# Kernel tuning notes

Measured on AMD Instinct MI355X. Metric: run time of the kernel, lower is better.

The kernel has to match this reference:

```python
import jax, jax.numpy as jnp
import numpy as np

N_NODES = 20000
N_EDGES = 320000
N_ADJ = 4
D = 256
CSTR = [0, 1]          # constrained adjacency subset for the last step
RATIO = 1.0
LN_EPS = 1e-5


def setup_inputs() -> dict:
    key = jax.random.key(0)
    ks = jax.random.split(key, 10)
    x = jax.random.normal(ks[0], (N_NODES, D), dtype=jnp.float32)
    rows = jax.random.randint(ks[1], (N_ADJ, N_EDGES), 0, N_NODES)
    cols = jax.random.randint(ks[2], (N_ADJ, N_EDGES), 0, N_NODES)
    vals = jax.random.uniform(ks[3], (N_ADJ, N_EDGES), dtype=jnp.float32)
    W = jax.random.normal(ks[4], (D, D), dtype=jnp.float32) * (1.0 / np.sqrt(D))
    b = jax.random.normal(ks[5], (D,), dtype=jnp.float32) * 0.02
    ws_seq_0 = jax.random.uniform(ks[6], (2, N_ADJ - 1), dtype=jnp.float32)
    ws_seq_1 = jax.random.uniform(ks[7], (len(CSTR),), dtype=jnp.float32)
    ws_res_0 = jax.random.uniform(ks[8], (1, N_ADJ), dtype=jnp.float32)
    ws_res_1 = jax.random.uniform(ks[9], (2, len(CSTR) + 1), dtype=jnp.float32)
    return {"x": x, "rows": rows, "cols": cols, "vals": vals, "W": W, "b": b,
            "ws_seq_0": ws_seq_0, "ws_seq_1": ws_seq_1,
            "ws_res_0": ws_res_0, "ws_res_1": ws_res_1}


def reference(x, rows, cols, vals, W, b, ws_seq_0, ws_seq_1, ws_res_0, ws_res_1):
    n_nodes = x.shape[0]

    def spmm(a, h):
        # sparse [n,n] @ h : gather source features, scale, scatter-add by row
        return jax.ops.segment_sum(vals[a][:, None] * h[cols[a]], rows[a],
                                   num_segments=n_nodes)

    def op(h, adj_ids, w):
        # Op with k=1: random.sample selects ALL operators -> weighted mean
        acc = w[0] * spmm(adj_ids[0], h)
        for j, a in enumerate(adj_ids[1:], start=1):
            acc = acc + w[j] * spmm(a, h)
        return acc / len(adj_ids)

    h = x @ W + b                      # affine: [n_nodes, D]
    states = [h]
    # step i=0: seq only (res sum over states[:0] is empty -> 0), edge == 1
    s1 = op(states[0], [0, 1, 2], ws_seq_0[0])          # adjs[:-1]
    states.append(s1)
    # step i=1: seq on states[1] over adjs[:-1], res on states[0] over all adjs
    s2 = op(states[1], [0, 1, 2], ws_seq_0[1]) + RATIO * op(states[0], [0, 1, 2, 3], ws_res_0[0])
    states.append(s2)
    # last step: cstr adjacencies for seq; cstr + last adj for residuals
    out_seq = op(states[2], CSTR, ws_seq_1)
    res_ids = CSTR + [N_ADJ - 1]
    out_res = op(states[0], res_ids, ws_res_1[0]) + op(states[1], res_ids, ws_res_1[1])
    out = out_seq + RATIO * out_res
    # LayerNorm without affine params
    mu = jnp.mean(out, axis=-1, keepdims=True)
    var = jnp.var(out, axis=-1, keepdims=True)
    out = (out - mu) * jax.lax.rsqrt(var + LN_EPS)
    return jax.nn.gelu(out, approximate=False)
```

## Files before the change

kernel.cpp:

```cpp
#include <hip/hip_runtime.h>
#include <hip/hip_bf16.h>

#define N_NODES 20000
#define N_EDGES 320000
#define N_ADJ   4
#define D       256
#define DH      128
#define RPA     20004

#define NBUCK   79
#define NGRP    40
#define EPB     8000
#define GCAP    192
#define BMAX    4736

typedef __attribute__((ext_vector_type(8))) short bf8;
typedef __attribute__((ext_vector_type(4))) float f4;


__device__ __forceinline__ unsigned f2bf_bits(float x) {
    unsigned u = __float_as_uint(x);
    return (u + 0x7FFFu + ((u >> 16) & 1u)) >> 16;
}
__device__ __forceinline__ unsigned pack_bf2(float lo, float hi) {
    return f2bf_bits(lo) | (f2bf_bits(hi) << 16);
}
__device__ __forceinline__ float bf_lo(unsigned p) { return __uint_as_float(p << 16); }
__device__ __forceinline__ float bf_hi(unsigned p) { return __uint_as_float(p & 0xFFFF0000u); }


__global__ __launch_bounds__(1024) void append_kernel(const int* __restrict__ rows,
                                                      const int* __restrict__ cols,
                                                      const float* __restrict__ vals,
                                                      int* __restrict__ cnt,
                                                      uint2* __restrict__ stage) {
    __shared__ int lcnt[NBUCK];
    int g = blockIdx.x, a = blockIdx.y, t = threadIdx.x;
    if (t < NBUCK) lcnt[t] = 0;
    __syncthreads();
    int e0 = g * EPB;
    #pragma unroll 1
    for (int i = 0; i < EPB; i += 1024) {
        int e = e0 + i + t;
        if (i + t < EPB) {
            int r   = rows[a * N_EDGES + e];
            int c   = cols[a * N_EDGES + e];
            float v = vals[a * N_EDGES + e];
            int b   = r >> 8;
            int idx = atomicAdd(&lcnt[b], 1);
            if (idx < GCAP) {
                stage[(size_t)((a * NBUCK + b) * NGRP + g) * GCAP + idx] =
                    make_uint2((f2bf_bits(v) << 16) | (unsigned)c, (unsigned)(r & 255));
            }
        }
    }
    __syncthreads();
    if (t < NBUCK) cnt[(a * NBUCK + t) * NGRP + g] = min(lcnt[t], GCAP);
}


__global__ __launch_bounds__(128) void bscan_kernel(const int* __restrict__ cnt,
                                                    int* __restrict__ bbase) {
    int a = blockIdx.x, t = threadIdx.x;
    __shared__ int buf[128];
    int tot = 0;
    if (t < NBUCK) {
        for (int g = 0; g < NGRP; ++g) tot += cnt[(a * NBUCK + t) * NGRP + g];
    }
    buf[t] = tot;
    __syncthreads();
    for (int off = 1; off < 128; off <<= 1) {
        int add = (t >= off) ? buf[t - off] : 0;
        __syncthreads();
        buf[t] += add;
        __syncthreads();
    }
    if (t < NBUCK) bbase[a * 80 + t] = buf[t] - tot;
}


__global__ __launch_bounds__(256) void bsort_kernel(const int* __restrict__ cnt,
                                                    const int* __restrict__ bbase,
                                                    const uint2* __restrict__ stage,
                                                    unsigned* __restrict__ csr,
                                                    int* __restrict__ row_ptr) {
    __shared__ uint2 recs[BMAX];
    __shared__ int scn[256];
    __shared__ int offs[256];
    int b = blockIdx.x, a = blockIdx.y, t = threadIdx.x;

    int goff = 0;
    #pragma unroll 1
    for (int g = 0; g < NGRP; ++g) {
        int c = cnt[(a * NBUCK + b) * NGRP + g];
        const uint2* src = stage + (size_t)((a * NBUCK + b) * NGRP + g) * GCAP;
        for (int i = t; i < c; i += 256) {
            int d = goff + i;
            if (d < BMAX) recs[d] = src[i];
        }
        goff += c;
    }
    int total = min(goff, BMAX);

    scn[t] = 0;
    offs[t] = 0;
    __syncthreads();
    for (int i = t; i < total; i += 256) atomicAdd(&scn[recs[i].y], 1);
    __syncthreads();
    int mycnt = scn[t];
    for (int off = 1; off < 256; off <<= 1) {
        int add = (t >= off) ? scn[t - off] : 0;
        __syncthreads();
        scn[t] += add;
        __syncthreads();
    }
    int excl = scn[t] - mycnt;
    __syncthreads();
    scn[t] = excl;
    __syncthreads();

    int gbase = bbase[a * 80 + b];
    for (int i = t; i < total; i += 256) {
        int lr  = recs[i].y;
        int pos = scn[lr] + atomicAdd(&offs[lr], 1);
        csr[(size_t)a * N_EDGES + gbase + pos] = recs[i].x;
    }
    int r = b * 256 + t;
    if (r <= N_NODES) row_ptr[(size_t)a * RPA + r] = gbase + excl;
}


__global__ __launch_bounds__(256) void wfrag_kernel(const float* __restrict__ W,
                                                    uint4* __restrict__ wh,
                                                    uint4* __restrict__ wl) {
    int g = blockIdx.x * 256 + threadIdx.x;
    int lane = g & 63;
    int tile = g >> 6;
    int ks = tile >> 4, n = tile & 15;
    int m = lane & 15, quad = lane >> 4;
    int col = n * 16 + m;
    int k0  = ks * 32 + quad * 8;
    unsigned hbits[8], lbits[8];
    #pragma unroll
    for (int j = 0; j < 8; ++j) {
        float v = W[(k0 + j) * D + col];
        unsigned hb = f2bf_bits(v);
        float lo = v - __uint_as_float(hb << 16);
        hbits[j] = hb;
        lbits[j] = f2bf_bits(lo);
    }
    uint4 hh, ll;
    hh.x = hbits[0] | (hbits[1] << 16); hh.y = hbits[2] | (hbits[3] << 16);
    hh.z = hbits[4] | (hbits[5] << 16); hh.w = hbits[6] | (hbits[7] << 16);
    ll.x = lbits[0] | (lbits[1] << 16); ll.y = lbits[2] | (lbits[3] << 16);
    ll.z = lbits[4] | (lbits[5] << 16); ll.w = lbits[6] | (lbits[7] << 16);
    wh[g] = hh;
    wl[g] = ll;
}


__global__ __launch_bounds__(256) void mfma_matmul_kernel(const float* __restrict__ x,
                                                          const uint4* __restrict__ wh,
                                                          const uint4* __restrict__ wl,
                                                          const float* __restrict__ b,
                                                          unsigned* __restrict__ hp) {
    __shared__ uint4 lbuf[2][1024];
    int t = threadIdx.x, wid = t >> 6, lane = t & 63;
    int r0 = (blockIdx.x * 4 + wid) * 16;
    bool active = r0 < N_NODES;
    int m = lane & 15, quad = lane >> 4;

    bf8 ah[8], al[8];
    if (active) {
        const float* xr = x + (size_t)(r0 + m) * D + quad * 8;
        #pragma unroll
        for (int ks = 0; ks < 8; ++ks) {
            float4 v0 = *(const float4*)(xr + ks * 32);
            float4 v1 = *(const float4*)(xr + ks * 32 + 4);
            float xs[8] = {v0.x, v0.y, v0.z, v0.w, v1.x, v1.y, v1.z, v1.w};
            #pragma unroll
            for (int j = 0; j < 8; ++j) {
                unsigned hb = f2bf_bits(xs[j]);
                float lo = xs[j] - __uint_as_float(hb << 16);
                ah[ks][j] = (short)hb;
                al[ks][j] = (short)f2bf_bits(lo);
            }
        }
    }

    #pragma unroll
    for (int j = 0; j < 4; ++j) {
        int idx = j * 256 + t;
        int ks = idx >> 7, hl = (idx >> 6) & 1, ln = idx & 63;
        lbuf[0][idx] = (hl ? wl : wh)[(ks * 16 + 0) * 64 + ln];
    }
    __syncthreads();

    for (int n = 0; n < 16; ++n) {
        int cur = n & 1, nxt = cur ^ 1;
        uint4 pre[4];
        if (n < 15) {
            #pragma unroll
            for (int j = 0; j < 4; ++j) {
                int idx = j * 256 + t;
                int ks = idx >> 7, hl = (idx >> 6) & 1, ln = idx & 63;
                pre[j] = (hl ? wl : wh)[(ks * 16 + (n + 1)) * 64 + ln];
            }
        }
        if (active) {
            f4 c = {0.f, 0.f, 0.f, 0.f};
            #pragma unroll
            for (int ks = 0; ks < 8; ++ks) {
                bf8 bh = *(bf8*)&lbuf[cur][ks * 128 + lane];
                bf8 bl = *(bf8*)&lbuf[cur][ks * 128 + 64 + lane];
                c = __builtin_amdgcn_mfma_f32_16x16x32_bf16(ah[ks], bh, c, 0, 0, 0);
                c = __builtin_amdgcn_mfma_f32_16x16x32_bf16(al[ks], bh, c, 0, 0, 0);
                c = __builtin_amdgcn_mfma_f32_16x16x32_bf16(ah[ks], bl, c, 0, 0, 0);
            }
            int col = n * 16 + m;
            float bb = b[col];
            #pragma unroll
            for (int reg = 0; reg < 4; ++reg) {
                float v = c[reg] + bb;
                float o = __shfl_xor(v, 1, 64);
                if ((m & 1) == 0) {
                    hp[(r0 + quad * 4 + reg) * DH + (col >> 1)] = pack_bf2(v, o);
                }
            }
        }
        if (n < 15) {
            __syncthreads();
            #pragma unroll
            for (int j = 0; j < 4; ++j) lbuf[nxt][j * 256 + t] = pre[j];
            __syncthreads();
        }
    }
}


__device__ __forceinline__ void gather_seg(const unsigned* __restrict__ E, int beg, int end,
                                           const uint2* __restrict__ feat2, int lane,
                                           float* __restrict__ s ) {
    int n = end - beg;
    const unsigned* e = E + beg;
    int m8 = n & ~7;
    if (m8) {
        unsigned rec[8];
        #pragma unroll
        for (int j = 0; j < 8; ++j) rec[j] = e[j];
        for (int i = 8; ; i += 8) {
            uint2 p[8];
            #pragma unroll
            for (int j = 0; j < 8; ++j)
                p[j] = feat2[((rec[j] & 0xFFFFu) << 6) + lane];
            bool more = i < m8;
            unsigned nrec[8];
            if (more) {
                #pragma unroll
                for (int j = 0; j < 8; ++j) nrec[j] = e[i + j];
            }
            #pragma unroll
            for (int j = 0; j < 8; ++j) {
                float v = __uint_as_float(rec[j] & 0xFFFF0000u);
                s[0] += v * bf_lo(p[j].x);
                s[1] += v * bf_hi(p[j].x);
                s[2] += v * bf_lo(p[j].y);
                s[3] += v * bf_hi(p[j].y);
            }
            if (!more) break;
            #pragma unroll
            for (int j = 0; j < 8; ++j) rec[j] = nrec[j];
        }
    }
    for (int i = m8; i < n; ++i) {
        unsigned rr = e[i];
        uint2 pp = feat2[((rr & 0xFFFFu) << 6) + lane];
        float vv = __uint_as_float(rr & 0xFFFF0000u);
        s[0] += vv * bf_lo(pp.x);
        s[1] += vv * bf_hi(pp.x);
        s[2] += vv * bf_lo(pp.y);
        s[3] += vv * bf_hi(pp.y);
    }
}


__global__ __launch_bounds__(256) void stage1_kernel(const uint2* __restrict__ hp2,
                                                     const int* __restrict__ row_ptr,
                                                     const unsigned* __restrict__ csr,
                                                     const float* __restrict__ wseq0,
                                                     const float* __restrict__ wres0,
                                                     const float* __restrict__ wres1,
                                                     uint2* __restrict__ s1p2,
                                                     uint2* __restrict__ s2p2,
                                                     float4* __restrict__ outp4) {
    int t = threadIdx.x, wid = t >> 6, lane = t & 63;
    int r = blockIdx.x * 4 + wid;
    float acc[N_ADJ][4];
    #pragma unroll
    for (int a = 0; a < N_ADJ; ++a) {
        acc[a][0] = acc[a][1] = acc[a][2] = acc[a][3] = 0.f;
        const int* rp = row_ptr + (size_t)a * RPA;
        int beg = __builtin_amdgcn_readfirstlane(rp[r]);
        int end = __builtin_amdgcn_readfirstlane(rp[r + 1]);
        gather_seg(csr + (size_t)a * N_EDGES, beg, end, hp2, lane, acc[a]);
    }
    const float third = 1.f / 3.f;
    float w0 = wseq0[0] * third, w1 = wseq0[1] * third, w2 = wseq0[2] * third;
    float q0 = wres0[0] * 0.25f, q1 = wres0[1] * 0.25f, q2 = wres0[2] * 0.25f, q3 = wres0[3] * 0.25f;
    float u0 = wres1[0] * third, u1 = wres1[1] * third, u2 = wres1[2] * third;
    float s1v[4], s2v[4], ov[4];
    #pragma unroll
    for (int j = 0; j < 4; ++j) {
        s1v[j] = w0 * acc[0][j] + w1 * acc[1][j] + w2 * acc[2][j];
        s2v[j] = q0 * acc[0][j] + q1 * acc[1][j] + q2 * acc[2][j] + q3 * acc[3][j];
        ov[j]  = u0 * acc[0][j] + u1 * acc[1][j] + u2 * acc[3][j];
    }
    int o = r * 64 + lane;
    s1p2[o]  = make_uint2(pack_bf2(s1v[0], s1v[1]), pack_bf2(s1v[2], s1v[3]));
    s2p2[o]  = make_uint2(pack_bf2(s2v[0], s2v[1]), pack_bf2(s2v[2], s2v[3]));
    outp4[o] = make_float4(ov[0], ov[1], ov[2], ov[3]);
}


__global__ __launch_bounds__(256) void stage2_kernel(const uint2* __restrict__ s1p2,
                                                     const int* __restrict__ row_ptr,
                                                     const unsigned* __restrict__ csr,
                                                     const float* __restrict__ wseq0,
                                                     const float* __restrict__ wres1,
                                                     uint2* __restrict__ s2p2,
                                                     float4* __restrict__ outp4) {
    int t = threadIdx.x, wid = t >> 6, lane = t & 63;
    int r = blockIdx.x * 4 + wid;
    float acc[N_ADJ][4];
    #pragma unroll
    for (int a = 0; a < N_ADJ; ++a) {
        acc[a][0] = acc[a][1] = acc[a][2] = acc[a][3] = 0.f;
        const int* rp = row_ptr + (size_t)a * RPA;
        int beg = __builtin_amdgcn_readfirstlane(rp[r]);
        int end = __builtin_amdgcn_readfirstlane(rp[r + 1]);
        gather_seg(csr + (size_t)a * N_EDGES, beg, end, s1p2, lane, acc[a]);
    }
    const float third = 1.f / 3.f;
    float w3 = wseq0[3] * third, w4 = wseq0[4] * third, w5 = wseq0[5] * third;
    float u3 = wres1[3] * third, u4 = wres1[4] * third, u5 = wres1[5] * third;
    int o = r * 64 + lane;
    uint2 sp = s2p2[o];
    float c0 = bf_lo(sp.x) + w3 * acc[0][0] + w4 * acc[1][0] + w5 * acc[2][0];
    float c1 = bf_hi(sp.x) + w3 * acc[0][1] + w4 * acc[1][1] + w5 * acc[2][1];
    float c2 = bf_lo(sp.y) + w3 * acc[0][2] + w4 * acc[1][2] + w5 * acc[2][2];
    float c3 = bf_hi(sp.y) + w3 * acc[0][3] + w4 * acc[1][3] + w5 * acc[2][3];
    s2p2[o] = make_uint2(pack_bf2(c0, c1), pack_bf2(c2, c3));
    float4 op = outp4[o];
    op.x += u3 * acc[0][0] + u4 * acc[1][0] + u5 * acc[3][0];
    op.y += u3 * acc[0][1] + u4 * acc[1][1] + u5 * acc[3][1];
    op.z += u3 * acc[0][2] + u4 * acc[1][2] + u5 * acc[3][2];
    op.w += u3 * acc[0][3] + u4 * acc[1][3] + u5 * acc[3][3];
    outp4[o] = op;
}


__global__ __launch_bounds__(256) void stage3_kernel(const uint2* __restrict__ s2p2,
                                                     const int* __restrict__ row_ptr,
                                                     const unsigned* __restrict__ csr,
                                                     const float* __restrict__ wseq1,
                                                     float4* __restrict__ outp4) {
    int t = threadIdx.x, wid = t >> 6, lane = t & 63;
    int r = blockIdx.x * 4 + wid;
    float acc[2][4];
    #pragma unroll
    for (int a = 0; a < 2; ++a) {
        acc[a][0] = acc[a][1] = acc[a][2] = acc[a][3] = 0.f;
        const int* rp = row_ptr + (size_t)a * RPA;
        int beg = __builtin_amdgcn_readfirstlane(rp[r]);
        int end = __builtin_amdgcn_readfirstlane(rp[r + 1]);
        gather_seg(csr + (size_t)a * N_EDGES, beg, end, s2p2, lane, acc[a]);
    }
    float e0 = wseq1[0] * 0.5f, e1 = wseq1[1] * 0.5f;
    int o = r * 64 + lane;
    float4 op = outp4[o];
    float v0 = op.x + e0 * acc[0][0] + e1 * acc[1][0];
    float v1 = op.y + e0 * acc[0][1] + e1 * acc[1][1];
    float v2 = op.z + e0 * acc[0][2] + e1 * acc[1][2];
    float v3 = op.w + e0 * acc[0][3] + e1 * acc[1][3];

    float sv = v0 + v1 + v2 + v3;
    float sq = v0 * v0 + v1 * v1 + v2 * v2 + v3 * v3;
    #pragma unroll
    for (int off = 32; off > 0; off >>= 1) {
        sv += __shfl_xor(sv, off, 64);
        sq += __shfl_xor(sq, off, 64);
    }
    float mu   = sv * (1.f / 256.f);
    float var  = sq * (1.f / 256.f) - mu * mu;
    float rstd = rsqrtf(var + 1e-5f);
    float y0 = (v0 - mu) * rstd;
    float y1 = (v1 - mu) * rstd;
    float y2 = (v2 - mu) * rstd;
    float y3 = (v3 - mu) * rstd;
    const float is2 = 0.70710678118654752440f;
    outp4[o] = make_float4(0.5f * y0 * (1.f + erff(y0 * is2)),
                           0.5f * y1 * (1.f + erff(y1 * is2)),
                           0.5f * y2 * (1.f + erff(y2 * is2)),
                           0.5f * y3 * (1.f + erff(y3 * is2)));
}


extern "C" void kernel_launch(void* const* d_in, const int* in_sizes, int n_in,
                              void* d_out, int out_size, void* d_ws, size_t ws_size,
                              hipStream_t stream) {
    const float* x     = (const float*)d_in[0];
    const int*   rows  = (const int*)d_in[1];
    const int*   cols  = (const int*)d_in[2];
    const float* vals  = (const float*)d_in[3];
    const float* W     = (const float*)d_in[4];
    const float* b     = (const float*)d_in[5];
    const float* wseq0 = (const float*)d_in[6];
    const float* wseq1 = (const float*)d_in[7];
    const float* wres0 = (const float*)d_in[8];
    const float* wres1 = (const float*)d_in[9];
    float4* outp4 = (float4*)d_out;

    char* p = (char*)d_ws;
    unsigned* hp  = (unsigned*)p; p += (size_t)N_NODES * DH * 4;
    unsigned* s1p = (unsigned*)p; p += (size_t)N_NODES * DH * 4;
    unsigned* s2p = (unsigned*)p; p += (size_t)N_NODES * DH * 4;
    int* row_ptr  = (int*)p;      p += (size_t)N_ADJ * RPA * 4;
    int* cnt      = (int*)p;      p += (N_ADJ * NBUCK * NGRP * 4 + 127) / 128 * 128;
    int* bbase    = (int*)p;      p += N_ADJ * 80 * 4;
    uint4* wh     = (uint4*)p;    p += 8192 * 16;
    uint4* wl     = (uint4*)p;    p += 8192 * 16;
    unsigned* csr = (unsigned*)p;
    uint2* stage  = (uint2*)s1p;

    append_kernel<<<dim3(NGRP, N_ADJ), 1024, 0, stream>>>(rows, cols, vals, cnt, stage);
    bscan_kernel<<<N_ADJ, 128, 0, stream>>>(cnt, bbase);
    bsort_kernel<<<dim3(NBUCK, N_ADJ), 256, 0, stream>>>(cnt, bbase, stage, csr, row_ptr);

    wfrag_kernel<<<32, 256, 0, stream>>>(W, wh, wl);
    mfma_matmul_kernel<<<313, 256, 0, stream>>>(x, wh, wl, b, hp);

    stage1_kernel<<<N_NODES / 4, 256, 0, stream>>>((const uint2*)hp, row_ptr, csr,
                                                   wseq0, wres0, wres1,
                                                   (uint2*)s1p, (uint2*)s2p, outp4);
    stage2_kernel<<<N_NODES / 4, 256, 0, stream>>>((const uint2*)s1p, row_ptr, csr,
                                                   wseq0, wres1, (uint2*)s2p, outp4);
    stage3_kernel<<<N_NODES / 4, 256, 0, stream>>>((const uint2*)s2p, row_ptr, csr,
                                                   wseq1, outp4);
}
```

Before: 348.6 us.

## Bin CSR edges by source-column chunk and gather chunk-by-chunk across adjacencies

The bucket sort now orders each row's edges by a 4-way source-column chunk and stores four per-row chunk offsets in an int4 row pointer. The stage kernels walk chunk by chunk across all adjacencies, so concurrent waves gather from a narrower slice of the feature matrix at a time, which is meant to improve L2 locality. The scalar remainder loop in the gather is also unrolled to issue up to seven loads at once. In exchange there are more short segments per row with their own tail handling, a larger row-pointer array, and larger shared histograms in the sort.

```diff
diff --git a/kernel.cpp b/kernel.cpp
--- a/kernel.cpp
+++ b/kernel.cpp
@@ -13,6 +13,7 @@
 #define EPB     8000
 #define GCAP    192
 #define BMAX    4736
+#define NCHUNK  4
 
 typedef __attribute__((ext_vector_type(8))) short bf8;
 typedef __attribute__((ext_vector_type(4))) float f4;
@@ -47,10 +48,12 @@
             int c   = cols[a * N_EDGES + e];
             float v = vals[a * N_EDGES + e];
             int b   = r >> 8;
+            int ch  = c / 5000;
             int idx = atomicAdd(&lcnt[b], 1);
             if (idx < GCAP) {
                 stage[(size_t)((a * NBUCK + b) * NGRP + g) * GCAP + idx] =
-                    make_uint2((f2bf_bits(v) << 16) | (unsigned)c, (unsigned)(r & 255));
+                    make_uint2((f2bf_bits(v) << 16) | (unsigned)c,
+                               (unsigned)((r & 255) | (ch << 8)));
             }
         }
     }
@@ -83,10 +86,11 @@
                                                     const int* __restrict__ bbase,
                                                     const uint2* __restrict__ stage,
                                                     unsigned* __restrict__ csr,
-                                                    int* __restrict__ row_ptr) {
+                                                    int4* __restrict__ row_ptr2) {
     __shared__ uint2 recs[BMAX];
+    __shared__ int binb[1024];
+    __shared__ int offs[1024];
     __shared__ int scn[256];
-    __shared__ int offs[256];
     int b = blockIdx.x, a = blockIdx.y, t = threadIdx.x;
 
     int goff = 0;
@@ -102,31 +106,40 @@
     }
     int total = min(goff, BMAX);
 
-    scn[t] = 0;
-    offs[t] = 0;
-    __syncthreads();
-    for (int i = t; i < total; i += 256) atomicAdd(&scn[recs[i].y], 1);
-    __syncthreads();
-    int mycnt = scn[t];
+    #pragma unroll
+    for (int j = 0; j < 4; ++j) { binb[t * 4 + j] = 0; offs[t * 4 + j] = 0; }
+    __syncthreads();
+    for (int i = t; i < total; i += 256) {
+        unsigned y = recs[i].y;
+        atomicAdd(&binb[(y & 255u) * 4 + (y >> 8)], 1);
+    }
+    __syncthreads();
+    int c0 = binb[t * 4], c1 = binb[t * 4 + 1], c2 = binb[t * 4 + 2], c3 = binb[t * 4 + 3];
+    int ts = c0 + c1 + c2 + c3;
+    scn[t] = ts;
+    __syncthreads();
     for (int off = 1; off < 256; off <<= 1) {
         int add = (t >= off) ? scn[t - off] : 0;
         __syncthreads();
         scn[t] += add;
         __syncthreads();
     }
-    int excl = scn[t] - mycnt;
-    __syncthreads();
-    scn[t] = excl;
+    int e0 = scn[t] - ts;
+    int e1 = e0 + c0, e2 = e1 + c1, e3 = e2 + c2;
+    binb[t * 4] = e0; binb[t * 4 + 1] = e1; binb[t * 4 + 2] = e2; binb[t * 4 + 3] = e3;
     __syncthreads();
 
     int gbase = bbase[a * 80 + b];
     for (int i = t; i < total; i += 256) {
-        int lr  = recs[i].y;
-        int pos = scn[lr] + atomicAdd(&offs[lr], 1);
+        unsigned y = recs[i].y;
+        int bin = (y & 255u) * 4 + (y >> 8);
+        int pos = binb[bin] + atomicAdd(&offs[bin], 1);
         csr[(size_t)a * N_EDGES + gbase + pos] = recs[i].x;
     }
     int r = b * 256 + t;
-    if (r <= N_NODES) row_ptr[(size_t)a * RPA + r] = gbase + excl;
+    if (r <= N_NODES)
+        row_ptr2[(size_t)a * RPA + r] =
+            make_int4(gbase + e0, gbase + e1, gbase + e2, gbase + e3);
 }
 
 
@@ -272,20 +285,26 @@
             for (int j = 0; j < 8; ++j) rec[j] = nrec[j];
         }
     }
-    for (int i = m8; i < n; ++i) {
-        unsigned rr = e[i];
-        uint2 pp = feat2[((rr & 0xFFFFu) << 6) + lane];
-        float vv = __uint_as_float(rr & 0xFFFF0000u);
-        s[0] += vv * bf_lo(pp.x);
-        s[1] += vv * bf_hi(pp.x);
-        s[2] += vv * bf_lo(pp.y);
-        s[3] += vv * bf_hi(pp.y);
+    int rem = n - m8;
+    unsigned rec[7];
+    uint2 p[7];
+    #pragma unroll
+    for (int j = 0; j < 7; ++j) if (j < rem) rec[j] = e[m8 + j];
+    #pragma unroll
+    for (int j = 0; j < 7; ++j) if (j < rem) p[j] = feat2[((rec[j] & 0xFFFFu) << 6) + lane];
+    #pragma unroll
+    for (int j = 0; j < 7; ++j) if (j < rem) {
+        float v = __uint_as_float(rec[j] & 0xFFFF0000u);
+        s[0] += v * bf_lo(p[j].x);
+        s[1] += v * bf_hi(p[j].x);
+        s[2] += v * bf_lo(p[j].y);
+        s[3] += v * bf_hi(p[j].y);
     }
 }
 
 
 __global__ __launch_bounds__(256) void stage1_kernel(const uint2* __restrict__ hp2,
-                                                     const int* __restrict__ row_ptr,
+                                                     const int4* __restrict__ row_ptr2,
                                                      const unsigned* __restrict__ csr,
                                                      const float* __restrict__ wseq0,
                                                      const float* __restrict__ wres0,
@@ -295,14 +314,29 @@
                                                      float4* __restrict__ outp4) {
     int t = threadIdx.x, wid = t >> 6, lane = t & 63;
     int r = blockIdx.x * 4 + wid;
+    int b0[N_ADJ], b1[N_ADJ], b2[N_ADJ], b3[N_ADJ], b4[N_ADJ];
+    #pragma unroll
+    for (int a = 0; a < N_ADJ; ++a) {
+        const int4* rp = row_ptr2 + (size_t)a * RPA;
+        int4 cu = rp[r];
+        b0[a] = __builtin_amdgcn_readfirstlane(cu.x);
+        b1[a] = __builtin_amdgcn_readfirstlane(cu.y);
+        b2[a] = __builtin_amdgcn_readfirstlane(cu.z);
+        b3[a] = __builtin_amdgcn_readfirstlane(cu.w);
+        b4[a] = __builtin_amdgcn_readfirstlane(rp[r + 1].x);
+    }
     float acc[N_ADJ][4];
     #pragma unroll
-    for (int a = 0; a < N_ADJ; ++a) {
+    for (int a = 0; a < N_ADJ; ++a)
         acc[a][0] = acc[a][1] = acc[a][2] = acc[a][3] = 0.f;
-        const int* rp = row_ptr + (size_t)a * RPA;
-        int beg = __builtin_amdgcn_readfirstlane(rp[r]);
-        int end = __builtin_amdgcn_readfirstlane(rp[r + 1]);
-        gather_seg(csr + (size_t)a * N_EDGES, beg, end, hp2, lane, acc[a]);
+    #pragma unroll
+    for (int c = 0; c < NCHUNK; ++c) {
+        #pragma unroll
+        for (int a = 0; a < N_ADJ; ++a) {
+            int beg = (c == 0) ? b0[a] : (c == 1) ? b1[a] : (c == 2) ? b2[a] : b3[a];
+            int end = (c == 0) ? b1[a] : (c == 1) ? b2[a] : (c == 2) ? b3[a] : b4[a];
+            gather_seg(csr + (size_t)a * N_EDGES, beg, end, hp2, lane, acc[a]);
+        }
     }
     const float third = 1.f / 3.f;
     float w0 = wseq0[0] * third, w1 = wseq0[1] * third, w2 = wseq0[2] * third;
@@ -323,7 +357,7 @@
 
 
 __global__ __launch_bounds__(256) void stage2_kernel(const uint2* __restrict__ s1p2,
-                                                     const int* __restrict__ row_ptr,
+                                                     const int4* __restrict__ row_ptr2,
                                                      const unsigned* __restrict__ csr,
                                                      const float* __restrict__ wseq0,
                                                      const float* __restrict__ wres1,
@@ -331,14 +365,29 @@
                                                      float4* __restrict__ outp4) {
     int t = threadIdx.x, wid = t >> 6, lane = t & 63;
     int r = blockIdx.x * 4 + wid;
+    int b0[N_ADJ], b1[N_ADJ], b2[N_ADJ], b3[N_ADJ], b4[N_ADJ];
+    #pragma unroll
+    for (int a = 0; a < N_ADJ; ++a) {
+        const int4* rp = row_ptr2 + (size_t)a * RPA;
+        int4 cu = rp[r];
+        b0[a] = __builtin_amdgcn_readfirstlane(cu.x);
+        b1[a] = __builtin_amdgcn_readfirstlane(cu.y);
+        b2[a] = __builtin_amdgcn_readfirstlane(cu.z);
+        b3[a] = __builtin_amdgcn_readfirstlane(cu.w);
+        b4[a] = __builtin_amdgcn_readfirstlane(rp[r + 1].x);
+    }
     float acc[N_ADJ][4];
     #pragma unroll
-    for (int a = 0; a < N_ADJ; ++a) {
+    for (int a = 0; a < N_ADJ; ++a)
         acc[a][0] = acc[a][1] = acc[a][2] = acc[a][3] = 0.f;
-        const int* rp = row_ptr + (size_t)a * RPA;
-        int beg = __builtin_amdgcn_readfirstlane(rp[r]);
-        int end = __builtin_amdgcn_readfirstlane(rp[r + 1]);
-        gather_seg(csr + (size_t)a * N_EDGES, beg, end, s1p2, lane, acc[a]);
+    #pragma unroll
+    for (int c = 0; c < NCHUNK; ++c) {
+        #pragma unroll
+        for (int a = 0; a < N_ADJ; ++a) {
+            int beg = (c == 0) ? b0[a] : (c == 1) ? b1[a] : (c == 2) ? b2[a] : b3[a];
+            int end = (c == 0) ? b1[a] : (c == 1) ? b2[a] : (c == 2) ? b3[a] : b4[a];
+            gather_seg(csr + (size_t)a * N_EDGES, beg, end, s1p2, lane, acc[a]);
+        }
     }
     const float third = 1.f / 3.f;
     float w3 = wseq0[3] * third, w4 = wseq0[4] * third, w5 = wseq0[5] * third;
@@ -360,20 +409,35 @@
 
 
 __global__ __launch_bounds__(256) void stage3_kernel(const uint2* __restrict__ s2p2,
-                                                     const int* __restrict__ row_ptr,
+                                                     const int4* __restrict__ row_ptr2,
                                                      const unsigned* __restrict__ csr,
                                                      const float* __restrict__ wseq1,
                                                      float4* __restrict__ outp4) {
     int t = threadIdx.x, wid = t >> 6, lane = t & 63;
     int r = blockIdx.x * 4 + wid;
+    int b0[2], b1[2], b2[2], b3[2], b4[2];
+    #pragma unroll
+    for (int a = 0; a < 2; ++a) {
+        const int4* rp = row_ptr2 + (size_t)a * RPA;
+        int4 cu = rp[r];
+        b0[a] = __builtin_amdgcn_readfirstlane(cu.x);
+        b1[a] = __builtin_amdgcn_readfirstlane(cu.y);
+        b2[a] = __builtin_amdgcn_readfirstlane(cu.z);
+        b3[a] = __builtin_amdgcn_readfirstlane(cu.w);
+        b4[a] = __builtin_amdgcn_readfirstlane(rp[r + 1].x);
+    }
     float acc[2][4];
     #pragma unroll
-    for (int a = 0; a < 2; ++a) {
+    for (int a = 0; a < 2; ++a)
         acc[a][0] = acc[a][1] = acc[a][2] = acc[a][3] = 0.f;
-        const int* rp = row_ptr + (size_t)a * RPA;
-        int beg = __builtin_amdgcn_readfirstlane(rp[r]);
-        int end = __builtin_amdgcn_readfirstlane(rp[r + 1]);
-        gather_seg(csr + (size_t)a * N_EDGES, beg, end, s2p2, lane, acc[a]);
+    #pragma unroll
+    for (int c = 0; c < NCHUNK; ++c) {
+        #pragma unroll
+        for (int a = 0; a < 2; ++a) {
+            int beg = (c == 0) ? b0[a] : (c == 1) ? b1[a] : (c == 2) ? b2[a] : b3[a];
+            int end = (c == 0) ? b1[a] : (c == 1) ? b2[a] : (c == 2) ? b3[a] : b4[a];
+            gather_seg(csr + (size_t)a * N_EDGES, beg, end, s2p2, lane, acc[a]);
+        }
     }
     float e0 = wseq1[0] * 0.5f, e1 = wseq1[1] * 0.5f;
     int o = r * 64 + lane;
@@ -421,29 +485,29 @@
     float4* outp4 = (float4*)d_out;
 
     char* p = (char*)d_ws;
-    unsigned* hp  = (unsigned*)p; p += (size_t)N_NODES * DH * 4;
-    unsigned* s1p = (unsigned*)p; p += (size_t)N_NODES * DH * 4;
-    unsigned* s2p = (unsigned*)p; p += (size_t)N_NODES * DH * 4;
-    int* row_ptr  = (int*)p;      p += (size_t)N_ADJ * RPA * 4;
-    int* cnt      = (int*)p;      p += (N_ADJ * NBUCK * NGRP * 4 + 127) / 128 * 128;
-    int* bbase    = (int*)p;      p += N_ADJ * 80 * 4;
-    uint4* wh     = (uint4*)p;    p += 8192 * 16;
-    uint4* wl     = (uint4*)p;    p += 8192 * 16;
-    unsigned* csr = (unsigned*)p;
-    uint2* stage  = (uint2*)s1p;
+    unsigned* hp   = (unsigned*)p; p += (size_t)N_NODES * DH * 4;
+    unsigned* s1p  = (unsigned*)p; p += (size_t)N_NODES * DH * 4;
+    unsigned* s2p  = (unsigned*)p; p += (size_t)N_NODES * DH * 4;
+    int4* row_ptr2 = (int4*)p;     p += (size_t)N_ADJ * RPA * 16;
+    int* cnt       = (int*)p;      p += (N_ADJ * NBUCK * NGRP * 4 + 127) / 128 * 128;
+    int* bbase     = (int*)p;      p += N_ADJ * 80 * 4;
+    uint4* wh      = (uint4*)p;    p += 8192 * 16;
+    uint4* wl      = (uint4*)p;    p += 8192 * 16;
+    unsigned* csr  = (unsigned*)p;
+    uint2* stage   = (uint2*)s1p;
 
     append_kernel<<<dim3(NGRP, N_ADJ), 1024, 0, stream>>>(rows, cols, vals, cnt, stage);
     bscan_kernel<<<N_ADJ, 128, 0, stream>>>(cnt, bbase);
-    bsort_kernel<<<dim3(NBUCK, N_ADJ), 256, 0, stream>>>(cnt, bbase, stage, csr, row_ptr);
+    bsort_kernel<<<dim3(NBUCK, N_ADJ), 256, 0, stream>>>(cnt, bbase, stage, csr, row_ptr2);
 
     wfrag_kernel<<<32, 256, 0, stream>>>(W, wh, wl);
     mfma_matmul_kernel<<<313, 256, 0, stream>>>(x, wh, wl, b, hp);
 
-    stage1_kernel<<<N_NODES / 4, 256, 0, stream>>>((const uint2*)hp, row_ptr, csr,
+    stage1_kernel<<<N_NODES / 4, 256, 0, stream>>>((const uint2*)hp, row_ptr2, csr,
                                                    wseq0, wres0, wres1,
                                                    (uint2*)s1p, (uint2*)s2p, outp4);
-    stage2_kernel<<<N_NODES / 4, 256, 0, stream>>>((const uint2*)s1p, row_ptr, csr,
+    stage2_kernel<<<N_NODES / 4, 256, 0, stream>>>((const uint2*)s1p, row_ptr2, csr,
                                                    wseq0, wres1, (uint2*)s2p, outp4);
-    stage3_kernel<<<N_NODES / 4, 256, 0, stream>>>((const uint2*)s2p, row_ptr, csr,
+    stage3_kernel<<<N_NODES / 4, 256, 0, stream>>>((const uint2*)s2p, row_ptr2, csr,
                                                    wseq1, outp4);
 }
```

After: 453.8 us. +30.2%, slower.

## Split matmul work across waves by output columns and drop LDS staging

Applied to the files above, without the earlier changes.

The affine matmul kernel now gives each block 16 rows, and each of its 4 waves computes 4 of the 16 output column tiles. B fragments are read straight from global/L2 instead of being double-buffered through LDS with block barriers. The grid grows from 313 to 1250 blocks, which spreads work more evenly over the CUs and removes the __syncthreads cost. In exchange, each wave reloads and re-splits the same x rows, so x traffic and conversion work rise about fourfold. The matmul is a small part of the whole pipeline.

```diff
diff --git a/kernel.cpp b/kernel.cpp
--- a/kernel.cpp
+++ b/kernel.cpp
@@ -164,75 +164,49 @@
                                                           const uint4* __restrict__ wl,
                                                           const float* __restrict__ b,
                                                           unsigned* __restrict__ hp) {
-    __shared__ uint4 lbuf[2][1024];
     int t = threadIdx.x, wid = t >> 6, lane = t & 63;
-    int r0 = (blockIdx.x * 4 + wid) * 16;
-    bool active = r0 < N_NODES;
+    int r0 = blockIdx.x * 16;
     int m = lane & 15, quad = lane >> 4;
 
+    const float* xr = x + (size_t)(r0 + m) * D + quad * 8;
     bf8 ah[8], al[8];
-    if (active) {
-        const float* xr = x + (size_t)(r0 + m) * D + quad * 8;
+    #pragma unroll
+    for (int ks = 0; ks < 8; ++ks) {
+        float4 v0 = *(const float4*)(xr + ks * 32);
+        float4 v1 = *(const float4*)(xr + ks * 32 + 4);
+        float xs[8] = {v0.x, v0.y, v0.z, v0.w, v1.x, v1.y, v1.z, v1.w};
+        #pragma unroll
+        for (int j = 0; j < 8; ++j) {
+            unsigned hb = f2bf_bits(xs[j]);
+            float lo = xs[j] - __uint_as_float(hb << 16);
+            ah[ks][j] = (short)hb;
+            al[ks][j] = (short)f2bf_bits(lo);
+        }
+    }
+
+    #pragma unroll
+    for (int i = 0; i < 4; ++i) {
+        int n = wid * 4 + i;
+        f4 c = {0.f, 0.f, 0.f, 0.f};
         #pragma unroll
         for (int ks = 0; ks < 8; ++ks) {
-            float4 v0 = *(const float4*)(xr + ks * 32);
-            float4 v1 = *(const float4*)(xr + ks * 32 + 4);
-            float xs[8] = {v0.x, v0.y, v0.z, v0.w, v1.x, v1.y, v1.z, v1.w};
-            #pragma unroll
-            for (int j = 0; j < 8; ++j) {
-                unsigned hb = f2bf_bits(xs[j]);
-                float lo = xs[j] - __uint_as_float(hb << 16);
-                ah[ks][j] = (short)hb;
-                al[ks][j] = (short)f2bf_bits(lo);
+            uint4 bh4 = wh[(ks * 16 + n) * 64 + lane];
+            uint4 bl4 = wl[(ks * 16 + n) * 64 + lane];
+            bf8 bh = *(bf8*)&bh4;
+            bf8 bl = *(bf8*)&bl4;
+            c = __builtin_amdgcn_mfma_f32_16x16x32_bf16(ah[ks], bh, c, 0, 0, 0);
+            c = __builtin_amdgcn_mfma_f32_16x16x32_bf16(al[ks], bh, c, 0, 0, 0);
+            c = __builtin_amdgcn_mfma_f32_16x16x32_bf16(ah[ks], bl, c, 0, 0, 0);
+        }
+        int col = n * 16 + m;
+        float bb = b[col];
+        #pragma unroll
+        for (int reg = 0; reg < 4; ++reg) {
+            float v = c[reg] + bb;
+            float o = __shfl_xor(v, 1, 64);
+            if ((m & 1) == 0) {
+                hp[(r0 + quad * 4 + reg) * DH + (col >> 1)] = pack_bf2(v, o);
             }
-        }
-    }
-
-    #pragma unroll
-    for (int j = 0; j < 4; ++j) {
-        int idx = j * 256 + t;
-        int ks = idx >> 7, hl = (idx >> 6) & 1, ln = idx & 63;
-        lbuf[0][idx] = (hl ? wl : wh)[(ks * 16 + 0) * 64 + ln];
-    }
-    __syncthreads();
-
-    for (int n = 0; n < 16; ++n) {
-        int cur = n & 1, nxt = cur ^ 1;
-        uint4 pre[4];
-        if (n < 15) {
-            #pragma unroll
-            for (int j = 0; j < 4; ++j) {
-                int idx = j * 256 + t;
-                int ks = idx >> 7, hl = (idx >> 6) & 1, ln = idx & 63;
-                pre[j] = (hl ? wl : wh)[(ks * 16 + (n + 1)) * 64 + ln];
-            }
-        }
-        if (active) {
-            f4 c = {0.f, 0.f, 0.f, 0.f};
-            #pragma unroll
-            for (int ks = 0; ks < 8; ++ks) {
-                bf8 bh = *(bf8*)&lbuf[cur][ks * 128 + lane];
-                bf8 bl = *(bf8*)&lbuf[cur][ks * 128 + 64 + lane];
-                c = __builtin_amdgcn_mfma_f32_16x16x32_bf16(ah[ks], bh, c, 0, 0, 0);
-                c = __builtin_amdgcn_mfma_f32_16x16x32_bf16(al[ks], bh, c, 0, 0, 0);
-                c = __builtin_amdgcn_mfma_f32_16x16x32_bf16(ah[ks], bl, c, 0, 0, 0);
-            }
-            int col = n * 16 + m;
-            float bb = b[col];
-            #pragma unroll
-            for (int reg = 0; reg < 4; ++reg) {
-                float v = c[reg] + bb;
-                float o = __shfl_xor(v, 1, 64);
-                if ((m & 1) == 0) {
-                    hp[(r0 + quad * 4 + reg) * DH + (col >> 1)] = pack_bf2(v, o);
-                }
-            }
-        }
-        if (n < 15) {
-            __syncthreads();
-            #pragma unroll
-            for (int j = 0; j < 4; ++j) lbuf[nxt][j * 256 + t] = pre[j];
-            __syncthreads();
         }
     }
 }
@@ -437,7 +411,7 @@
     bsort_kernel<<<dim3(NBUCK, N_ADJ), 256, 0, stream>>>(cnt, bbase, stage, csr, row_ptr);
 
     wfrag_kernel<<<32, 256, 0, stream>>>(W, wh, wl);
-    mfma_matmul_kernel<<<313, 256, 0, stream>>>(x, wh, wl, b, hp);
+    mfma_matmul_kernel<<<1250, 256, 0, stream>>>(x, wh, wl, b, hp);
 
     stage1_kernel<<<N_NODES / 4, 256, 0, stream>>>((const uint2*)hp, row_ptr, csr,
                                                    wseq0, wres0, wres1,
```

After: 330.7 us. -5.1%, faster.
